# Kernel tuning notes

Hardware: AMD Instinct MI355X
Metric: run time of the kernel (lower is better)

The kernel has to match this reference:

```python
import jax, jax.numpy as jnp
import numpy as np

HEADS = 4
SPARSITY_WEIGHT = 0.1
LN_EPS = 1e-5


def setup_inputs() -> dict:
    key = jax.random.key(0)
    ks = jax.random.split(key, 6)
    b, n, d = 4, 2048, 512
    x = jax.random.normal(ks[0], (b, n, d), dtype=jnp.float32)
    alibi_bias = jax.random.normal(ks[1], (b, n, n), dtype=jnp.float32)
    gamma = jax.random.normal(ks[2], (b, d), dtype=jnp.float32)
    beta = jax.random.normal(ks[3], (b, d), dtype=jnp.float32)
    ln_w = jnp.ones((d,), dtype=jnp.float32)
    ln_b = jnp.zeros((d,), dtype=jnp.float32)
    w_qkv = jax.random.normal(ks[4], (d, 3 * d), dtype=jnp.float32) * (d ** -0.5)
    w_out = jax.random.normal(ks[5], (d, d), dtype=jnp.float32) * (d ** -0.5)
    return {"x": x, "alibi_bias": alibi_bias, "gamma": gamma, "beta": beta,
            "ln_w": ln_w, "ln_b": ln_b, "w_qkv": w_qkv, "w_out": w_out}


def reference(x, alibi_bias, gamma, beta, ln_w, ln_b, w_qkv, w_out):
    b, n, d = x.shape
    dh = d // HEADS
    scale = dh ** -0.5
    # LayerNorm over last dim
    mu = jnp.mean(x, axis=-1, keepdims=True)
    var = jnp.mean(jnp.square(x - mu), axis=-1, keepdims=True)
    xn = (x - mu) * jax.lax.rsqrt(var + LN_EPS) * ln_w + ln_b
    # FiLM
    xn = gamma[:, None, :] * xn + beta[:, None, :]
    # QKV projection (Linear, no bias)
    qkv = xn @ w_qkv  # [b, n, 3d]
    q, k, v = jnp.split(qkv, 3, axis=-1)
    split_heads = lambda t: t.reshape(b, n, HEADS, dh).transpose(0, 2, 1, 3)  # b h n d
    q, k, v = split_heads(q), split_heads(k), split_heads(v)
    dots = jnp.einsum('bhid,bhjd->bhij', q, k) * scale
    dots = dots + alibi_bias[:, None, :, :]  # broadcast over heads
    attn = jax.nn.softmax(dots, axis=-1)
    eps = 1e-8
    entropy = -(attn * jnp.log(attn + eps)).sum(axis=-1)
    sparsity_loss = entropy.mean() * SPARSITY_WEIGHT
    out = jnp.einsum('bhij,bhjd->bhid', attn, v)
    out = out.transpose(0, 2, 1, 3).reshape(b, n, d)
    return out @ w_out, sparsity_loss
```

## Files before the change

kernel.cpp:

```cpp
#include <hip/hip_runtime.h>
#include <hip/hip_bf16.h>

typedef __attribute__((ext_vector_type(8))) short short8;
typedef __attribute__((ext_vector_type(4))) float f32x4;

static constexpr int NN = 2048, DD = 512;
static constexpr float SCALE = 0.088388347648318447f;
static constexpr float ENT_SCALE = 0.1f / 32768.0f;

__device__ __forceinline__ short f2bf(float f) {
  __hip_bfloat16 h = __float2bfloat16(f);
  return *reinterpret_cast<short*>(&h);
}

__device__ __forceinline__ void async_cp16(const void* g, void* l) {
  __builtin_amdgcn_global_load_lds((const __attribute__((address_space(1))) void*)g,
                                   (__attribute__((address_space(3))) void*)l, 16, 0, 0);
}

__global__ __launch_bounds__(256) void ln_film_k(
    const float* __restrict__ x, const float* __restrict__ gamma,
    const float* __restrict__ beta, const float* __restrict__ lnw,
    const float* __restrict__ lnb, short* __restrict__ xn) {
  const int wave = threadIdx.x >> 6, lane = threadIdx.x & 63;
  const int row = blockIdx.x * 4 + wave;
  const int b = row >> 11;
  const float4* xr = reinterpret_cast<const float4*>(x + (size_t)row * DD);
  float4 u = xr[lane * 2], v = xr[lane * 2 + 1];
  float s  = u.x + u.y + u.z + u.w + v.x + v.y + v.z + v.w;
  float ss = u.x*u.x + u.y*u.y + u.z*u.z + u.w*u.w + v.x*v.x + v.y*v.y + v.z*v.z + v.w*v.w;
  #pragma unroll
  for (int m = 1; m < 64; m <<= 1) { s += __shfl_xor(s, m); ss += __shfl_xor(ss, m); }
  const float mu = s * (1.0f / DD);
  const float rs = rsqrtf(ss * (1.0f / DD) - mu * mu + 1e-5f);
  const int c0 = lane * 8;
  float vals[8] = {u.x,u.y,u.z,u.w,v.x,v.y,v.z,v.w};
  short8 o;
  #pragma unroll
  for (int i = 0; i < 8; ++i) {
    const int c = c0 + i;
    const float t = (vals[i] - mu) * rs * lnw[c] + lnb[c];
    o[i] = f2bf(gamma[b * DD + c] * t + beta[b * DD + c]);
  }
  *reinterpret_cast<short8*>(xn + (size_t)row * DD + c0) = o;
}

__global__ void transpose_bf16_k(const float* __restrict__ w, short* __restrict__ wt,
                                 int K, int Nc) {
  const int id = blockIdx.x * 256 + threadIdx.x;
  if (id >= K * Nc) return;
  const int k = id / Nc, c = id - k * Nc;
  wt[(size_t)c * K + k] = f2bf(w[id]);
}

template<int NT, bool BF16OUT>
__global__ __launch_bounds__(256) void gemm_bt_k(
    const short* __restrict__ A, const short* __restrict__ Bt, void* __restrict__ C) {
  constexpr int K = 512;
  __shared__ char lds[32768];
  char* const Alds = lds;
  char* const Blds = lds + 16384;
  constexpr int nTiles = NT / 128;
  const int m0 = (blockIdx.x / nTiles) * 128;
  const int n0 = (blockIdx.x % nTiles) * 128;
  const int tid = threadIdx.x, wave = tid >> 6, lane = tid & 63;
  const int wm = wave >> 1, wn = wave & 1;
  const int lg = lane >> 4, li = lane & 15;
  f32x4 acc[4][4] = {};
  for (int kt = 0; kt < K / 64; ++kt) {
    __syncthreads();
    #pragma unroll
    for (int i = 0; i < 4; ++i) {
      const int chunk = wave * 4 + i;
      const int m = chunk * 8 + (lane >> 3);
      const int cs = ((lane & 7) * 16) ^ ((m & 7) << 4);
      async_cp16((const char*)A  + ((size_t)(m0 + m) * K + kt * 64) * 2 + cs, Alds + chunk * 1024);
      async_cp16((const char*)Bt + ((size_t)(n0 + m) * K + kt * 64) * 2 + cs, Blds + chunk * 1024);
    }
    __syncthreads();
    #pragma unroll
    for (int ks = 0; ks < 2; ++ks) {
      const int kb = ks * 64 + lg * 16;
      short8 af[4], bfr[4];
      #pragma unroll
      for (int t = 0; t < 4; ++t) {
        const int r = wm * 64 + t * 16 + li;
        af[t]  = *reinterpret_cast<const short8*>(Alds + r * 128 + (kb ^ ((r & 7) << 4)));
        const int c = wn * 64 + t * 16 + li;
        bfr[t] = *reinterpret_cast<const short8*>(Blds + c * 128 + (kb ^ ((c & 7) << 4)));
      }
      #pragma unroll
      for (int mt = 0; mt < 4; ++mt)
        #pragma unroll
        for (int nt = 0; nt < 4; ++nt)
          acc[mt][nt] = __builtin_amdgcn_mfma_f32_16x16x32_bf16(af[mt], bfr[nt], acc[mt][nt], 0, 0, 0);
    }
  }
  #pragma unroll
  for (int mt = 0; mt < 4; ++mt) {
    #pragma unroll
    for (int nt = 0; nt < 4; ++nt) {
      const int row = m0 + wm * 64 + mt * 16 + lg * 4;
      const int col = n0 + wn * 64 + nt * 16 + li;
      #pragma unroll
      for (int r = 0; r < 4; ++r) {
        if (BF16OUT)
          reinterpret_cast<short*>(C)[(size_t)(row + r) * NT + col] = f2bf(acc[mt][nt][r]);
        else
          reinterpret_cast<float*>(C)[(size_t)(row + r) * NT + col] = acc[mt][nt][r];
      }
    }
  }
}

__global__ __launch_bounds__(256) void attn_k(
    const short* __restrict__ qkv, const float* __restrict__ alibi,
    short* __restrict__ ao, float* __restrict__ ent) {
  __shared__ char Klds[16384];
  __shared__ char Vlds[16384];
  __shared__ short Plds[4][1024];
  const int qt = blockIdx.x, bh = blockIdx.y;
  const int b = bh >> 2, h = bh & 3;
  const int tid = threadIdx.x, wave = tid >> 6, lane = tid & 63;
  const int lg = lane >> 4, li = lane & 15;
  short* const Vs = reinterpret_cast<short*>(Vlds);

  const int qrow = qt * 64 + wave * 16 + li;
  const char* qptr = (const char*)qkv + ((size_t)(b * NN + qrow) * 1536 + h * 128) * 2;
  short8 qf[4];
  #pragma unroll
  for (int kq = 0; kq < 4; ++kq)
    qf[kq] = *reinterpret_cast<const short8*>(qptr + kq * 64 + lg * 16);

  f32x4 oacc[8] = {};
  float mrow[4], lrow[4], trow[4];
  #pragma unroll
  for (int r = 0; r < 4; ++r) { mrow[r] = -INFINITY; lrow[r] = 0.f; trow[r] = 0.f; }
  const float* arow = alibi + ((size_t)b * NN + (qt * 64 + wave * 16 + lg * 4)) * NN;

  for (int kt = 0; kt < 32; ++kt) {
    __syncthreads();
    #pragma unroll
    for (int i = 0; i < 4; ++i) {
      const int chunk = wave * 4 + i;
      const int mloc = chunk * 4 + lg;
      const int cs = (li * 16) ^ ((mloc & 7) << 4);
      const size_t src = ((size_t)(b * NN + kt * 64 + mloc) * 1536 + 512 + h * 128) * 2 + cs;
      async_cp16((const char*)qkv + src, Klds + chunk * 1024);
    }
    #pragma unroll
    for (int p = 0; p < 4; ++p) {
      const int dh0 = wave * 8 + p * 32;
      const int jv = lane;
      short8 vv = *reinterpret_cast<const short8*>(
          (const char*)qkv + ((size_t)(b * NN + kt * 64 + jv) * 1536 + 1024 + h * 128 + dh0) * 2);
      #pragma unroll
      for (int i2 = 0; i2 < 8; ++i2) {
        const int dh = dh0 + i2;
        Vs[dh * 64 + (jv ^ ((dh & 7) << 3))] = vv[i2];
      }
    }
    __syncthreads();
    f32x4 sacc[4] = {};
    #pragma unroll
    for (int ct = 0; ct < 4; ++ct) {
      const int key = ct * 16 + li;
      #pragma unroll
      for (int kq = 0; kq < 4; ++kq) {
        short8 kf = *reinterpret_cast<const short8*>(
            Klds + key * 256 + ((kq * 64 + lg * 16) ^ ((key & 7) << 4)));
        sacc[ct] = __builtin_amdgcn_mfma_f32_16x16x32_bf16(qf[kq], kf, sacc[ct], 0, 0, 0);
      }
    }
    float sv[4][4];
    #pragma unroll
    for (int ct = 0; ct < 4; ++ct)
      #pragma unroll
      for (int r = 0; r < 4; ++r)
        sv[ct][r] = sacc[ct][r] * SCALE + arow[(size_t)r * NN + kt * 64 + ct * 16 + li];
    #pragma unroll
    for (int r = 0; r < 4; ++r) {
      float mx = fmaxf(fmaxf(sv[0][r], sv[1][r]), fmaxf(sv[2][r], sv[3][r]));
      #pragma unroll
      for (int msk = 1; msk < 16; msk <<= 1) mx = fmaxf(mx, __shfl_xor(mx, msk, 16));
      const float newm = fmaxf(mrow[r], mx);
      const float fsc = __expf(mrow[r] - newm);
      float ps[4], lsum = 0.f, tsum = 0.f;
      #pragma unroll
      for (int ct = 0; ct < 4; ++ct) {
        ps[ct] = __expf(sv[ct][r] - newm);
        lsum += ps[ct];
        tsum += ps[ct] * sv[ct][r];
      }
      #pragma unroll
      for (int msk = 1; msk < 16; msk <<= 1) {
        lsum += __shfl_xor(lsum, msk, 16);
        tsum += __shfl_xor(tsum, msk, 16);
      }
      lrow[r] = lrow[r] * fsc + lsum;
      trow[r] = trow[r] * fsc + tsum;
      mrow[r] = newm;
      #pragma unroll
      for (int nt = 0; nt < 8; ++nt) oacc[nt][r] *= fsc;
      const int prow = lg * 4 + r;
      #pragma unroll
      for (int ct = 0; ct < 4; ++ct)
        Plds[wave][prow * 64 + ((ct * 16 + li) ^ ((prow & 7) << 3))] = f2bf(ps[ct]);
    }
    #pragma unroll
    for (int ks = 0; ks < 2; ++ks) {
      const int kb = ks * 64 + lg * 16;
      short8 pa = *reinterpret_cast<const short8*>(
          (const char*)Plds[wave] + li * 128 + (kb ^ ((li & 7) << 4)));
      #pragma unroll
      for (int nt = 0; nt < 8; ++nt) {
        const int dh = nt * 16 + li;
        short8 vb = *reinterpret_cast<const short8*>(
            Vlds + dh * 128 + (kb ^ ((dh & 7) << 4)));
        oacc[nt] = __builtin_amdgcn_mfma_f32_16x16x32_bf16(pa, vb, oacc[nt], 0, 0, 0);
      }
    }
  }
  const int orow = b * NN + qt * 64 + wave * 16 + lg * 4;
  #pragma unroll
  for (int nt = 0; nt < 8; ++nt)
    #pragma unroll
    for (int r = 0; r < 4; ++r)
      ao[(size_t)(orow + r) * DD + h * 128 + nt * 16 + li] = f2bf(oacc[nt][r] / lrow[r]);
  if (li == 0) {
    float e = 0.f;
    #pragma unroll
    for (int r = 0; r < 4; ++r) e += mrow[r] + logf(lrow[r]) - trow[r] / lrow[r];
    atomicAdd(ent, e * ENT_SCALE);
  }
}

extern "C" void kernel_launch(void* const* d_in, const int* in_sizes, int n_in,
                              void* d_out, int out_size, void* d_ws, size_t ws_size,
                              hipStream_t stream) {
  const float* x     = (const float*)d_in[0];
  const float* alibi = (const float*)d_in[1];
  const float* gamma = (const float*)d_in[2];
  const float* beta  = (const float*)d_in[3];
  const float* lnw   = (const float*)d_in[4];
  const float* lnb   = (const float*)d_in[5];
  const float* wqkv  = (const float*)d_in[6];
  const float* wout  = (const float*)d_in[7];
  float* out = (float*)d_out;

  char* ws = (char*)d_ws;
  short* xn    = (short*)(ws);
  short* wqkvT = (short*)(ws + 8388608);
  short* woutT = (short*)(ws + 8388608 + 1572864);
  short* qkv   = (short*)(ws + 10485760);
  short* ao    = (short*)(ws);

  hipMemsetAsync(out + 4194304, 0, 4, stream);
  ln_film_k<<<2048, 256, 0, stream>>>(x, gamma, beta, lnw, lnb, xn);
  transpose_bf16_k<<<(512 * 1536 + 255) / 256, 256, 0, stream>>>(wqkv, wqkvT, 512, 1536);
  transpose_bf16_k<<<(512 * 512 + 255) / 256, 256, 0, stream>>>(wout, woutT, 512, 512);
  gemm_bt_k<1536, true><<<64 * 12, 256, 0, stream>>>(xn, wqkvT, qkv);
  attn_k<<<dim3(32, 16), 256, 0, stream>>>(qkv, alibi, ao, out + 4194304);
  gemm_bt_k<512, false><<<64 * 4, 256, 0, stream>>>(ao, woutT, out);
}
```

Baseline: 303.1 us.

## Double-buffer GEMM and attention tiles, transpose score layout, add lazy softmax rescale

The GEMM kernel now double-buffers its A/B tiles in LDS and takes a templated M tile, which lets the output projection use 64-row tiles and launch more blocks. The attention kernel double-buffers K and V in LDS and prefetches the next V tile and the alibi bias into registers while the current tile is computed. It also swaps the MFMA operands so each lane owns a whole query row. That turns the alibi reads into contiguous float4 loads and lets row reductions use only two cross-lane shuffles. Rescaling is skipped unless a wave's max rises by more than a threshold, which trades more LDS space and registers for less latency and less rescale work.

Result: faster. 269.5 us (-11.1%).

```diff
diff --git a/kernel.cpp b/kernel.cpp
--- a/kernel.cpp
+++ b/kernel.cpp
@@ -2,6 +2,7 @@
 #include <hip/hip_bf16.h>
 
 typedef __attribute__((ext_vector_type(8))) short short8;
+typedef __attribute__((ext_vector_type(4))) short short4_t;
 typedef __attribute__((ext_vector_type(4))) float f32x4;
 
 static constexpr int NN = 2048, DD = 512;
@@ -53,54 +54,74 @@
   wt[(size_t)c * K + k] = f2bf(w[id]);
 }
 
-template<int NT, bool BF16OUT>
+template<int BM, int NT, bool BF16OUT>
 __global__ __launch_bounds__(256) void gemm_bt_k(
     const short* __restrict__ A, const short* __restrict__ Bt, void* __restrict__ C) {
   constexpr int K = 512;
-  __shared__ char lds[32768];
-  char* const Alds = lds;
-  char* const Blds = lds + 16384;
+  constexpr int ABYTES = BM * 128;
+  __shared__ char lds[2 * ABYTES + 32768];
   constexpr int nTiles = NT / 128;
-  const int m0 = (blockIdx.x / nTiles) * 128;
+  const int m0 = (blockIdx.x / nTiles) * BM;
   const int n0 = (blockIdx.x % nTiles) * 128;
   const int tid = threadIdx.x, wave = tid >> 6, lane = tid & 63;
   const int wm = wave >> 1, wn = wave & 1;
   const int lg = lane >> 4, li = lane & 15;
-  f32x4 acc[4][4] = {};
-  for (int kt = 0; kt < K / 64; ++kt) {
-    __syncthreads();
-    #pragma unroll
-    for (int i = 0; i < 4; ++i) {
-      const int chunk = wave * 4 + i;
-      const int m = chunk * 8 + (lane >> 3);
+  constexpr int MT = BM / 32;
+  f32x4 acc[MT][4] = {};
+
+  auto stage = [&](int buf, int kt) {
+    #pragma unroll
+    for (int t = 0; t < BM / 32; ++t) {
+      const int dbase = t * 4096 + wave * 1024;
+      const int m = (dbase >> 7) + (lane >> 3);
       const int cs = ((lane & 7) * 16) ^ ((m & 7) << 4);
-      async_cp16((const char*)A  + ((size_t)(m0 + m) * K + kt * 64) * 2 + cs, Alds + chunk * 1024);
-      async_cp16((const char*)Bt + ((size_t)(n0 + m) * K + kt * 64) * 2 + cs, Blds + chunk * 1024);
-    }
-    __syncthreads();
+      async_cp16((const char*)A + ((size_t)(m0 + m) * K + kt * 64) * 2 + cs,
+                 lds + buf * ABYTES + dbase);
+    }
+    #pragma unroll
+    for (int t = 0; t < 4; ++t) {
+      const int dbase = t * 4096 + wave * 1024;
+      const int n = (dbase >> 7) + (lane >> 3);
+      const int cs = ((lane & 7) * 16) ^ ((n & 7) << 4);
+      async_cp16((const char*)Bt + ((size_t)(n0 + n) * K + kt * 64) * 2 + cs,
+                 lds + 2 * ABYTES + buf * 16384 + dbase);
+    }
+  };
+
+  stage(0, 0);
+  __syncthreads();
+  for (int kt = 0; kt < 8; ++kt) {
+    const int cur = kt & 1;
+    if (kt < 7) stage(cur ^ 1, kt + 1);
+    const char* Al = lds + cur * ABYTES;
+    const char* Bl = lds + 2 * ABYTES + cur * 16384;
     #pragma unroll
     for (int ks = 0; ks < 2; ++ks) {
       const int kb = ks * 64 + lg * 16;
-      short8 af[4], bfr[4];
+      short8 af[MT], bfr[4];
+      #pragma unroll
+      for (int t = 0; t < MT; ++t) {
+        const int r = wm * (BM / 2) + t * 16 + li;
+        af[t] = *reinterpret_cast<const short8*>(Al + r * 128 + (kb ^ ((r & 7) << 4)));
+      }
       #pragma unroll
       for (int t = 0; t < 4; ++t) {
-        const int r = wm * 64 + t * 16 + li;
-        af[t]  = *reinterpret_cast<const short8*>(Alds + r * 128 + (kb ^ ((r & 7) << 4)));
         const int c = wn * 64 + t * 16 + li;
-        bfr[t] = *reinterpret_cast<const short8*>(Blds + c * 128 + (kb ^ ((c & 7) << 4)));
-      }
-      #pragma unroll
-      for (int mt = 0; mt < 4; ++mt)
+        bfr[t] = *reinterpret_cast<const short8*>(Bl + c * 128 + (kb ^ ((c & 7) << 4)));
+      }
+      #pragma unroll
+      for (int mt = 0; mt < MT; ++mt)
         #pragma unroll
         for (int nt = 0; nt < 4; ++nt)
           acc[mt][nt] = __builtin_amdgcn_mfma_f32_16x16x32_bf16(af[mt], bfr[nt], acc[mt][nt], 0, 0, 0);
     }
-  }
-  #pragma unroll
-  for (int mt = 0; mt < 4; ++mt) {
+    __syncthreads();
+  }
+  #pragma unroll
+  for (int mt = 0; mt < MT; ++mt) {
     #pragma unroll
     for (int nt = 0; nt < 4; ++nt) {
-      const int row = m0 + wm * 64 + mt * 16 + lg * 4;
+      const int row = m0 + wm * (BM / 2) + mt * 16 + lg * 4;
       const int col = n0 + wn * 64 + nt * 16 + li;
       #pragma unroll
       for (int r = 0; r < 4; ++r) {
@@ -116,14 +137,12 @@
 __global__ __launch_bounds__(256) void attn_k(
     const short* __restrict__ qkv, const float* __restrict__ alibi,
     short* __restrict__ ao, float* __restrict__ ent) {
-  __shared__ char Klds[16384];
-  __shared__ char Vlds[16384];
-  __shared__ short Plds[4][1024];
+  __shared__ char lds[73728];
   const int qt = blockIdx.x, bh = blockIdx.y;
   const int b = bh >> 2, h = bh & 3;
   const int tid = threadIdx.x, wave = tid >> 6, lane = tid & 63;
   const int lg = lane >> 4, li = lane & 15;
-  short* const Vs = reinterpret_cast<short*>(Vlds);
+  char* const Pbase = lds + 65536 + wave * 2048;
 
   const int qrow = qt * 64 + wave * 16 + li;
   const char* qptr = (const char*)qkv + ((size_t)(b * NN + qrow) * 1536 + h * 128) * 2;
@@ -133,106 +152,136 @@
     qf[kq] = *reinterpret_cast<const short8*>(qptr + kq * 64 + lg * 16);
 
   f32x4 oacc[8] = {};
-  float mrow[4], lrow[4], trow[4];
-  #pragma unroll
-  for (int r = 0; r < 4; ++r) { mrow[r] = -INFINITY; lrow[r] = 0.f; trow[r] = 0.f; }
-  const float* arow = alibi + ((size_t)b * NN + (qt * 64 + wave * 16 + lg * 4)) * NN;
-
-  for (int kt = 0; kt < 32; ++kt) {
-    __syncthreads();
+  float mrow = -INFINITY, lrow = 0.f, trow = 0.f;
+  const float* arow = alibi + (size_t)(b * NN + qrow) * NN;
+
+  auto stageK = [&](int buf, int kt) {
     #pragma unroll
     for (int i = 0; i < 4; ++i) {
       const int chunk = wave * 4 + i;
       const int mloc = chunk * 4 + lg;
       const int cs = (li * 16) ^ ((mloc & 7) << 4);
-      const size_t src = ((size_t)(b * NN + kt * 64 + mloc) * 1536 + 512 + h * 128) * 2 + cs;
-      async_cp16((const char*)qkv + src, Klds + chunk * 1024);
-    }
-    #pragma unroll
-    for (int p = 0; p < 4; ++p) {
-      const int dh0 = wave * 8 + p * 32;
-      const int jv = lane;
-      short8 vv = *reinterpret_cast<const short8*>(
-          (const char*)qkv + ((size_t)(b * NN + kt * 64 + jv) * 1536 + 1024 + h * 128 + dh0) * 2);
+      async_cp16((const char*)qkv + ((size_t)(b * NN + kt * 64 + mloc) * 1536 + 512 + h * 128) * 2 + cs,
+                 lds + buf * 16384 + chunk * 1024);
+    }
+  };
+  auto loadV = [&](int kt, short8* vv) {
+    #pragma unroll
+    for (int p = 0; p < 4; ++p)
+      vv[p] = *reinterpret_cast<const short8*>(
+          (const char*)qkv + ((size_t)(b * NN + kt * 64 + lane) * 1536 + 1024 + h * 128 + wave * 8 + p * 32) * 2);
+  };
+  auto writeV = [&](int buf, const short8* vv) {
+    short* Vp = reinterpret_cast<short*>(lds + 32768 + buf * 16384);
+    #pragma unroll
+    for (int p = 0; p < 4; ++p)
       #pragma unroll
       for (int i2 = 0; i2 < 8; ++i2) {
-        const int dh = dh0 + i2;
-        Vs[dh * 64 + (jv ^ ((dh & 7) << 3))] = vv[i2];
-      }
-    }
-    __syncthreads();
+        const int dh = wave * 8 + p * 32 + i2;
+        Vp[dh * 64 + (lane ^ ((dh & 7) << 3))] = vv[p][i2];
+      }
+  };
+  auto loadA = [&](int kt, float4* ab) {
+    #pragma unroll
+    for (int ct = 0; ct < 4; ++ct)
+      ab[ct] = *reinterpret_cast<const float4*>(arow + kt * 64 + ct * 16 + lg * 4);
+  };
+
+  short8 vv[4]; float4 ab[4];
+  stageK(0, 0); loadV(0, vv); loadA(0, ab);
+  writeV(0, vv);
+  __syncthreads();
+
+  for (int kt = 0; kt < 32; ++kt) {
+    const int cur = kt & 1, nxt = cur ^ 1;
+    short8 vvn[4]; float4 abn[4];
+    if (kt < 31) { stageK(nxt, kt + 1); loadV(kt + 1, vvn); loadA(kt + 1, abn); }
+
     f32x4 sacc[4] = {};
+    const char* Kl = lds + cur * 16384;
     #pragma unroll
     for (int ct = 0; ct < 4; ++ct) {
       const int key = ct * 16 + li;
       #pragma unroll
       for (int kq = 0; kq < 4; ++kq) {
         short8 kf = *reinterpret_cast<const short8*>(
-            Klds + key * 256 + ((kq * 64 + lg * 16) ^ ((key & 7) << 4)));
-        sacc[ct] = __builtin_amdgcn_mfma_f32_16x16x32_bf16(qf[kq], kf, sacc[ct], 0, 0, 0);
-      }
-    }
-    float sv[4][4];
+            Kl + key * 256 + ((kq * 64 + lg * 16) ^ ((key & 7) << 4)));
+        sacc[ct] = __builtin_amdgcn_mfma_f32_16x16x32_bf16(kf, qf[kq], sacc[ct], 0, 0, 0);
+      }
+    }
+    float sv[4][4], p[4][4];
+    #pragma unroll
+    for (int ct = 0; ct < 4; ++ct) {
+      sv[ct][0] = sacc[ct][0] * SCALE + ab[ct].x;
+      sv[ct][1] = sacc[ct][1] * SCALE + ab[ct].y;
+      sv[ct][2] = sacc[ct][2] * SCALE + ab[ct].z;
+      sv[ct][3] = sacc[ct][3] * SCALE + ab[ct].w;
+    }
+    float mx = sv[0][0];
     #pragma unroll
     for (int ct = 0; ct < 4; ++ct)
       #pragma unroll
-      for (int r = 0; r < 4; ++r)
-        sv[ct][r] = sacc[ct][r] * SCALE + arow[(size_t)r * NN + kt * 64 + ct * 16 + li];
-    #pragma unroll
-    for (int r = 0; r < 4; ++r) {
-      float mx = fmaxf(fmaxf(sv[0][r], sv[1][r]), fmaxf(sv[2][r], sv[3][r]));
-      #pragma unroll
-      for (int msk = 1; msk < 16; msk <<= 1) mx = fmaxf(mx, __shfl_xor(mx, msk, 16));
-      const float newm = fmaxf(mrow[r], mx);
-      const float fsc = __expf(mrow[r] - newm);
-      float ps[4], lsum = 0.f, tsum = 0.f;
-      #pragma unroll
-      for (int ct = 0; ct < 4; ++ct) {
-        ps[ct] = __expf(sv[ct][r] - newm);
-        lsum += ps[ct];
-        tsum += ps[ct] * sv[ct][r];
-      }
-      #pragma unroll
-      for (int msk = 1; msk < 16; msk <<= 1) {
-        lsum += __shfl_xor(lsum, msk, 16);
-        tsum += __shfl_xor(tsum, msk, 16);
-      }
-      lrow[r] = lrow[r] * fsc + lsum;
-      trow[r] = trow[r] * fsc + tsum;
-      mrow[r] = newm;
-      #pragma unroll
-      for (int nt = 0; nt < 8; ++nt) oacc[nt][r] *= fsc;
-      const int prow = lg * 4 + r;
-      #pragma unroll
-      for (int ct = 0; ct < 4; ++ct)
-        Plds[wave][prow * 64 + ((ct * 16 + li) ^ ((prow & 7) << 3))] = f2bf(ps[ct]);
-    }
+      for (int r = 0; r < 4; ++r) mx = fmaxf(mx, sv[ct][r]);
+    mx = fmaxf(mx, __shfl_xor(mx, 16));
+    mx = fmaxf(mx, __shfl_xor(mx, 32));
+    const bool resc = !__all(mx <= mrow + 8.0f);
+    float newm = mrow, fsc = 1.0f;
+    if (resc) { newm = fmaxf(mrow, mx); fsc = __expf(mrow - newm); }
+    float lsum = 0.f, tsum = 0.f;
+    #pragma unroll
+    for (int ct = 0; ct < 4; ++ct)
+      #pragma unroll
+      for (int r = 0; r < 4; ++r) {
+        p[ct][r] = __expf(sv[ct][r] - newm);
+        lsum += p[ct][r];
+        tsum = fmaf(p[ct][r], sv[ct][r], tsum);
+      }
+    lsum += __shfl_xor(lsum, 16); lsum += __shfl_xor(lsum, 32);
+    tsum += __shfl_xor(tsum, 16); tsum += __shfl_xor(tsum, 32);
+    if (resc) {
+      lrow = lrow * fsc + lsum; trow = trow * fsc + tsum; mrow = newm;
+      #pragma unroll
+      for (int nt = 0; nt < 8; ++nt) oacc[nt] *= fsc;
+    } else { lrow += lsum; trow += tsum; }
+    #pragma unroll
+    for (int ct = 0; ct < 4; ++ct) {
+      short4_t pw;
+      #pragma unroll
+      for (int r = 0; r < 4; ++r) pw[r] = f2bf(p[ct][r]);
+      *reinterpret_cast<short4_t*>(Pbase + li * 128 + ((ct * 32 + lg * 8) ^ ((li & 7) << 4))) = pw;
+    }
+    const char* Vl = lds + 32768 + cur * 16384;
     #pragma unroll
     for (int ks = 0; ks < 2; ++ks) {
       const int kb = ks * 64 + lg * 16;
-      short8 pa = *reinterpret_cast<const short8*>(
-          (const char*)Plds[wave] + li * 128 + (kb ^ ((li & 7) << 4)));
+      short8 pa = *reinterpret_cast<const short8*>(Pbase + li * 128 + (kb ^ ((li & 7) << 4)));
       #pragma unroll
       for (int nt = 0; nt < 8; ++nt) {
         const int dh = nt * 16 + li;
-        short8 vb = *reinterpret_cast<const short8*>(
-            Vlds + dh * 128 + (kb ^ ((dh & 7) << 4)));
-        oacc[nt] = __builtin_amdgcn_mfma_f32_16x16x32_bf16(pa, vb, oacc[nt], 0, 0, 0);
-      }
-    }
-  }
-  const int orow = b * NN + qt * 64 + wave * 16 + lg * 4;
-  #pragma unroll
-  for (int nt = 0; nt < 8; ++nt)
-    #pragma unroll
-    for (int r = 0; r < 4; ++r)
-      ao[(size_t)(orow + r) * DD + h * 128 + nt * 16 + li] = f2bf(oacc[nt][r] / lrow[r]);
-  if (li == 0) {
-    float e = 0.f;
-    #pragma unroll
-    for (int r = 0; r < 4; ++r) e += mrow[r] + logf(lrow[r]) - trow[r] / lrow[r];
-    atomicAdd(ent, e * ENT_SCALE);
-  }
+        short8 vb = *reinterpret_cast<const short8*>(Vl + dh * 128 + (kb ^ ((dh & 7) << 4)));
+        oacc[nt] = __builtin_amdgcn_mfma_f32_16x16x32_bf16(vb, pa, oacc[nt], 0, 0, 0);
+      }
+    }
+    if (kt < 31) {
+      writeV(nxt, vvn);
+      #pragma unroll
+      for (int ct = 0; ct < 4; ++ct) ab[ct] = abn[ct];
+    }
+    __syncthreads();
+  }
+
+  const float invl = 1.0f / lrow;
+  #pragma unroll
+  for (int nt = 0; nt < 8; ++nt) {
+    short4_t ow;
+    #pragma unroll
+    for (int r = 0; r < 4; ++r) ow[r] = f2bf(oacc[nt][r] * invl);
+    *reinterpret_cast<short4_t*>(ao + (size_t)(b * NN + qrow) * DD + h * 128 + nt * 16 + lg * 4) = ow;
+  }
+  float e = (lg == 0) ? (mrow + logf(lrow) - trow * invl) : 0.f;
+  #pragma unroll
+  for (int m = 1; m < 64; m <<= 1) e += __shfl_xor(e, m);
+  if (lane == 0) atomicAdd(ent, e * ENT_SCALE);
 }
 
 extern "C" void kernel_launch(void* const* d_in, const int* in_sizes, int n_in,
@@ -259,7 +308,7 @@
   ln_film_k<<<2048, 256, 0, stream>>>(x, gamma, beta, lnw, lnb, xn);
   transpose_bf16_k<<<(512 * 1536 + 255) / 256, 256, 0, stream>>>(wqkv, wqkvT, 512, 1536);
   transpose_bf16_k<<<(512 * 512 + 255) / 256, 256, 0, stream>>>(wout, woutT, 512, 512);
-  gemm_bt_k<1536, true><<<64 * 12, 256, 0, stream>>>(xn, wqkvT, qkv);
+  gemm_bt_k<128, 1536, true><<<64 * 12, 256, 0, stream>>>(xn, wqkvT, qkv);
   attn_k<<<dim3(32, 16), 256, 0, stream>>>(qkv, alibi, ao, out + 4194304);
-  gemm_bt_k<512, false><<<64 * 4, 256, 0, stream>>>(ao, woutT, out);
-}
+  gemm_bt_k<64, 512, false><<<128 * 4, 256, 0, stream>>>(ao, woutT, out);
+}
```
